# Optimization experiments

Hardware: AMD Instinct MI355X
Metric: run time of the kernel (lower is better)

Reference implementation:

```python
import jax, jax.numpy as jnp
import numpy as np

D_MODEL = 1024
D_STATE = 16
EXPAND = 2
D_INNER = D_MODEL * EXPAND          # 2048
DT_RANK = (D_MODEL + 15) // 16      # 64 (auto)
BATCH = 2
SEQ = 1024


def setup_inputs() -> dict:
    key = jax.random.key(0)
    ks = jax.random.split(key, 8)
    def nrm(k, shape, scale):
        return jax.random.normal(k, shape, dtype=jnp.float32) * scale
    x = jax.random.normal(ks[0], (BATCH, SEQ, D_MODEL), dtype=jnp.float32)
    W_in = nrm(ks[1], (D_MODEL, 2 * D_INNER), D_MODEL ** -0.5)
    W_conv = nrm(ks[2], (D_INNER, 3), 3 ** -0.5)           # depthwise kernel, taps [t-2,t-1,t]
    W_x = nrm(ks[3], (D_INNER, DT_RANK + 2 * D_STATE), D_INNER ** -0.5)
    W_dt = nrm(ks[4], (DT_RANK, D_INNER), DT_RANK ** -0.5)
    b_dt = nrm(ks[5], (D_INNER,), 0.1)
    # A_log init exactly as in the torch module: log(arange(1..d_state)) per channel
    A_log = jnp.log(jnp.tile(jnp.arange(1, D_STATE + 1, dtype=jnp.float32), (D_INNER, 1)))
    D_param = jnp.ones((D_INNER,), dtype=jnp.float32)
    W_out = nrm(ks[6], (D_INNER, D_MODEL), D_INNER ** -0.5)
    return {"x": x, "W_in": W_in, "W_conv": W_conv, "W_x": W_x,
            "W_dt": W_dt, "b_dt": b_dt, "A_log": A_log, "D_param": D_param,
            "W_out": W_out}


def _s6_forward(x, W_in, W_conv, W_x, W_dt, b_dt, A_log, D_param, W_out):
    B, L, _ = x.shape
    # input projection -> (u, res)
    u, res = jnp.split(x @ W_in, 2, axis=-1)           # each [B, L, d_inner]
    # depthwise causal conv, kernel=3, left pad 2 (matches Conv1d(pad=2)[..., :L])
    up = jnp.pad(u, ((0, 0), (2, 0), (0, 0)))
    u = (up[:, :L] * W_conv[:, 0]
         + up[:, 1:L + 1] * W_conv[:, 1]
         + up[:, 2:L + 2] * W_conv[:, 2])
    u = jax.nn.silu(u)
    # input-dependent SSM params
    x_dbl = u @ W_x                                     # [B, L, dt_rank + 2*d_state]
    dt, Bm, Cm = jnp.split(x_dbl, [DT_RANK, DT_RANK + D_STATE], axis=-1)
    delta = jax.nn.softplus(dt @ W_dt + b_dt)           # [B, L, d_inner]
    A = -jnp.exp(A_log)                                 # [d_inner, d_state]
    deltaA = jnp.exp(jnp.einsum('bld,dn->bldn', delta, A))     # [B, L, D, N]
    deltaB_u = jnp.einsum('bld,bln->bldn', delta * u, Bm)      # [B, L, D, N]
    # sequential selective scan over L via lax.scan
    def step(h, inp):
        dA, dbu, c = inp                # dA,dbu: [B,D,N], c: [B,N]
        h = dA * h + dbu
        y = jnp.einsum('bdn,bn->bd', h, c)
        return h, y
    h0 = jnp.zeros((B, D_INNER, D_STATE), dtype=u.dtype)
    _, ys = jax.lax.scan(step, h0, (jnp.moveaxis(deltaA, 1, 0),
                                    jnp.moveaxis(deltaB_u, 1, 0),
                                    jnp.moveaxis(Cm, 1, 0)))
    y = jnp.moveaxis(ys, 0, 1)                          # [B, L, d_inner]
    y = y + u * D_param
    y = y * jax.nn.silu(res)
    return y @ W_out                                    # [B, L, d_model]


def reference(x, W_in, W_conv, W_x, W_dt, b_dt, A_log, D_param, W_out):
    return _s6_forward(x, W_in, W_conv, W_x, W_dt, b_dt, A_log, D_param, W_out)
```

## Files before the change

kernel.cpp:

```cpp
#include <hip/hip_runtime.h>
#include <math.h>
#include <stdint.h>

#define BATCH 2
#define SEQ   1024
#define DM    1024
#define DI    2048
#define DS    16
#define DTR   64
#define ROWS  (BATCH*SEQ)
#define CH    32
#define NCH   (SEQ/CH)
#define NSPLIT 16
#define G4SPLIT 4

typedef unsigned short u16;
typedef __bf16 bf16x8 __attribute__((ext_vector_type(8)));
typedef float  f32x4  __attribute__((ext_vector_type(4)));
typedef short  short8 __attribute__((ext_vector_type(8)));
typedef short  short4v __attribute__((ext_vector_type(4)));

__device__ __forceinline__ float bf2f(u16 v) {
    return __uint_as_float(((unsigned)v) << 16);
}
__device__ __forceinline__ u16 f2bf(float f) {
    unsigned u = __float_as_uint(f);
    return (u16)((u + 0x7FFFu + ((u >> 16) & 1u)) >> 16);
}
__device__ __forceinline__ float softplus_f(float v) {
    return fmaxf(v, 0.f) + __logf(1.f + __expf(-fabsf(v)));
}
__device__ __forceinline__ float silu_f(float v) {
    return v / (1.f + __expf(-v));
}

__device__ __forceinline__ void gload16(const void* g, const void* l) {
    __builtin_amdgcn_global_load_lds(
        (const __attribute__((address_space(1))) unsigned int*)(uintptr_t)g,
        (__attribute__((address_space(3))) unsigned int*)(uintptr_t)l,
        16, 0, 0);
}

template<int EPI, typename TOUT>
__global__ __launch_bounds__(256) void gemm_bf16(
    const u16* __restrict__ A,
    const u16* __restrict__ BT,
    TOUT* __restrict__ C, u16* __restrict__ C2,
    int ldc, int N, int Ksplit, long long zCstride,
    const float* __restrict__ bias)
{
    __shared__ u16 As[2][128 * 64];
    __shared__ u16 Bs[2][128 * 64];

    const int K = (int)gridDim.z * Ksplit;
    int tid  = threadIdx.x;
    int lane = tid & 63, wid = tid >> 6;
    int wr = wid >> 1, wc = wid & 1;
    int row0 = blockIdx.y * 128, col0 = blockIdx.x * 128;
    int kbeg = blockIdx.z * Ksplit;
    const int niter = Ksplit >> 6;

    int sRow = wid * 32 + (lane >> 3);
    int sCol = (((lane & 7) ^ ((lane >> 3) & 7))) * 8;

    const u16* Abase = A  + (size_t)(row0 + sRow) * K + sCol;
    const u16* Bbase = BT + (size_t)(col0 + sRow) * K + sCol;

    int frow = lane & 15;
    int s0   = lane >> 4;
    int r7   = lane & 7;

    f32x4 acc[4][4] = {};

#define STAGE(buf, kk)                                                          \
    do {                                                                        \
        _Pragma("unroll")                                                       \
        for (int c = 0; c < 4; ++c) {                                           \
            gload16(Abase + (size_t)c * 8 * K + (kk),                           \
                    As[buf] + (wid * 32 + c * 8) * 64);                         \
            gload16(Bbase + (size_t)c * 8 * K + (kk),                           \
                    Bs[buf] + (wid * 32 + c * 8) * 64);                         \
        }                                                                       \
    } while (0)

    STAGE(0, kbeg);

    for (int i = 0; i < niter; ++i) {
        __syncthreads();
        int cur = i & 1;
        if (i + 1 < niter) STAGE(cur ^ 1, kbeg + (i + 1) * 64);

        #pragma unroll
        for (int kk = 0; kk < 2; ++kk) {
            bf16x8 af[4], bfr[4];
            #pragma unroll
            for (int m = 0; m < 4; ++m) {
                int row = wr * 64 + m * 16 + frow;
                int off = row * 64 + (((kk * 4 + s0) ^ r7) * 8);
                af[m] = *(const bf16x8*)(As[cur] + off);
            }
            #pragma unroll
            for (int n = 0; n < 4; ++n) {
                int row = wc * 64 + n * 16 + frow;
                int off = row * 64 + (((kk * 4 + s0) ^ r7) * 8);
                bfr[n] = *(const bf16x8*)(Bs[cur] + off);
            }
            #pragma unroll
            for (int m = 0; m < 4; ++m)
                #pragma unroll
                for (int n = 0; n < 4; ++n)
                    acc[m][n] = __builtin_amdgcn_mfma_f32_16x16x32_bf16(
                        af[m], bfr[n], acc[m][n], 0, 0, 0);
        }
    }
#undef STAGE

    int orow = row0 + wr * 64 + (lane >> 4) * 4;
    int ocol = col0 + wc * 64 + (lane & 15);

    if (EPI == 1) {
        bool isres = (col0 >= 2048);
        u16* dst = isres ? C2 : (u16*)C;
        int cb0 = ocol - (isres ? 2048 : 0);
        #pragma unroll
        for (int m = 0; m < 4; ++m)
            #pragma unroll
            for (int n = 0; n < 4; ++n) {
                int col = cb0 + n * 16;
                int roww = orow + m * 16;
                u16 tmp[4];
                #pragma unroll
                for (int r = 0; r < 4; ++r) {
                    float v = acc[m][n][r];
                    tmp[r] = f2bf(isres ? silu_f(v) : v);
                }
                *(short4v*)(dst + (size_t)col * ROWS + roww) = *(short4v*)tmp;
            }
    } else if (EPI == 2) {
        #pragma unroll
        for (int m = 0; m < 4; ++m)
            #pragma unroll
            for (int n = 0; n < 4; ++n) {
                int col = ocol + n * 16;
                int roww = orow + m * 16;
                float bv = bias[col];
                u16 tmp[4];
                #pragma unroll
                for (int r = 0; r < 4; ++r)
                    tmp[r] = f2bf(softplus_f(acc[m][n][r] + bv));
                *(short4v*)((u16*)C + (size_t)col * ROWS + roww) = *(short4v*)tmp;
            }
    } else {
        size_t zoff = (size_t)blockIdx.z * (size_t)zCstride;
        #pragma unroll
        for (int m = 0; m < 4; ++m)
            #pragma unroll
            for (int n = 0; n < 4; ++n) {
                int colb = ocol + n * 16;
                if (colb < N) {
                    #pragma unroll
                    for (int r = 0; r < 4; ++r) {
                        float v = acc[m][n][r];
                        size_t o = zoff + (size_t)(orow + m * 16 + r) * ldc + colb;
                        if constexpr (sizeof(TOUT) == 2) C[o] = (TOUT)f2bf(v);
                        else                             C[o] = (TOUT)v;
                    }
                }
            }
    }
}

__global__ __launch_bounds__(256) void tcast_kernel(
    const float* __restrict__ in, u16* __restrict__ outp,
    int K, int N, int Npad)
{
    __shared__ float tile[32][33];
    int tx = threadIdx.x & 31;
    int ty = threadIdx.x >> 5;
    int k0 = blockIdx.y * 32, n0 = blockIdx.x * 32;
    #pragma unroll
    for (int i = 0; i < 4; ++i) {
        int k = k0 + ty + i * 8, n = n0 + tx;
        tile[ty + i * 8][tx] = (k < K && n < N) ? in[(size_t)k * N + n] : 0.f;
    }
    __syncthreads();
    #pragma unroll
    for (int i = 0; i < 4; ++i) {
        int n = n0 + ty + i * 8, k = k0 + tx;
        if (n < Npad && k < K)
            outp[(size_t)n * K + k] = f2bf(tile[tx][ty + i * 8]);
    }
}

__global__ __launch_bounds__(256) void tbf_kernel(
    const u16* __restrict__ in, u16* __restrict__ outp, int R, int C)
{
    __shared__ u16 t[64][66];
    int tx = threadIdx.x & 63, ty = threadIdx.x >> 6;
    int r0 = blockIdx.y * 64, c0 = blockIdx.x * 64;
    #pragma unroll
    for (int i = 0; i < 16; ++i) {
        int r = ty + i * 4;
        t[r][tx] = in[(size_t)(r0 + r) * C + c0 + tx];
    }
    __syncthreads();
    #pragma unroll
    for (int i = 0; i < 16; ++i) {
        int r = ty + i * 4;
        outp[(size_t)(c0 + r) * R + r0 + tx] = t[tx][r];
    }
}

__global__ __launch_bounds__(256) void cast_kernel(
    const float* __restrict__ in, u16* __restrict__ outp, int n)
{
    int i = (blockIdx.x * 256 + threadIdx.x) * 4;
    if (i < n) {
        float4 v = *(const float4*)(in + i);
        outp[i + 0] = f2bf(v.x); outp[i + 1] = f2bf(v.y);
        outp[i + 2] = f2bf(v.z); outp[i + 3] = f2bf(v.w);
    }
}

__global__ __launch_bounds__(256) void reduce_split_kernel(
    const float* __restrict__ part, float* __restrict__ xdbl,
    u16* __restrict__ dtbf)
{
    int i = blockIdx.x * 256 + threadIdx.x;
    if (i < ROWS * 96) {
        float s = 0.f;
        #pragma unroll
        for (int z = 0; z < NSPLIT; ++z) s += part[(size_t)z * ROWS * 96 + i];
        xdbl[i] = s;
        int row = i / 96, col = i - row * 96;
        if (col < 64) dtbf[row * 64 + col] = f2bf(s);
    }
}

__global__ __launch_bounds__(256) void reduce4_kernel(
    const float* __restrict__ part, float* __restrict__ outp)
{
    int i = (blockIdx.x * 256 + threadIdx.x) * 4;
    const size_t S = (size_t)ROWS * 1024;
    float4 a = *(const float4*)(part + i);
    float4 b = *(const float4*)(part + S + i);
    float4 c = *(const float4*)(part + 2 * S + i);
    float4 d = *(const float4*)(part + 3 * S + i);
    float4 o;
    o.x = a.x + b.x + c.x + d.x;
    o.y = a.y + b.y + c.y + d.y;
    o.z = a.z + b.z + c.z + d.z;
    o.w = a.w + b.w + c.w + d.w;
    *(float4*)(outp + i) = o;
}

__global__ __launch_bounds__(256) void conv_silu_kernel(
    const u16* __restrict__ upreT,
    const float* __restrict__ Wc,
    u16* __restrict__ uT)
{
    int gt = blockIdx.x * 256 + threadIdx.x;
    int rb = gt & (ROWS / 8 - 1);
    int d  = gt >> 8;
    int r0 = rb * 8;
    int l0 = r0 & (SEQ - 1);
    const u16* rowp = upreT + (size_t)d * ROWS + r0;
    short8 cur = *(const short8*)rowp;
    float w0 = Wc[d * 3 + 0], w1 = Wc[d * 3 + 1], w2 = Wc[d * 3 + 2];
    float pm1 = (l0 > 0) ? bf2f(rowp[-1]) : 0.f;
    float pm2 = (l0 > 0) ? bf2f(rowp[-2]) : 0.f;
    float c[8];
    #pragma unroll
    for (int j = 0; j < 8; ++j) c[j] = bf2f((u16)cur[j]);
    short8 o;
    o[0] = (short)f2bf(silu_f(w2 * c[0] + w1 * pm1 + w0 * pm2));
    o[1] = (short)f2bf(silu_f(w2 * c[1] + w1 * c[0] + w0 * pm1));
    #pragma unroll
    for (int j = 2; j < 8; ++j)
        o[j] = (short)f2bf(silu_f(w2 * c[j] + w1 * c[j - 1] + w0 * c[j - 2]));
    *(short8*)(uT + (size_t)d * ROWS + r0) = o;
}

__global__ __launch_bounds__(256) void scan_chunk_kernel(
    const u16*  __restrict__ dvT,
    const u16*  __restrict__ uT,
    const float* __restrict__ xdbl,
    const float* __restrict__ A_log,
    float* __restrict__ P,
    float* __restrict__ Q)
{
    int gtid = blockIdx.x * 256 + threadIdx.x;
    int nq = gtid & 3;
    int d  = (gtid >> 2) & (DI - 1);
    int rc = gtid >> 13;
    int chunk = rc & (NCH - 1);
    int b = rc >> 5;

    float4 a4 = *(const float4*)(A_log + (size_t)d * DS + nq * 4);
    float Av[4] = {-__expf(a4.x), -__expf(a4.y), -__expf(a4.z), -__expf(a4.w)};
    float h[4] = {};
    float dsum = 0.f;

    int r0 = b * SEQ + chunk * CH;
    const u16* drow = dvT + (size_t)d * ROWS + r0;
    const u16* urow = uT  + (size_t)d * ROWS + r0;
    const float* xrow = xdbl + (size_t)r0 * 96 + 64 + nq * 4;

    #pragma unroll
    for (int half = 0; half < 2; ++half) {
        short8 dv8[2], u8[2];
        #pragma unroll
        for (int q = 0; q < 2; ++q) {
            dv8[q] = *(const short8*)(drow + half * 16 + q * 8);
            u8[q]  = *(const short8*)(urow + half * 16 + q * 8);
        }
        #pragma unroll
        for (int j = 0; j < 16; ++j) {
            int l = half * 16 + j;
            float dv = bf2f((u16)dv8[j >> 3][j & 7]);
            float du = dv * bf2f((u16)u8[j >> 3][j & 7]);
            dsum += dv;
            float4 b4 = *(const float4*)(xrow + l * 96);
            h[0] = __expf(dv * Av[0]) * h[0] + du * b4.x;
            h[1] = __expf(dv * Av[1]) * h[1] + du * b4.y;
            h[2] = __expf(dv * Av[2]) * h[2] + du * b4.z;
            h[3] = __expf(dv * Av[3]) * h[3] + du * b4.w;
        }
    }
    size_t off = ((size_t)(b * NCH + chunk) * DI + d) * DS + nq * 4;
    float4 p4 = {__expf(dsum * Av[0]), __expf(dsum * Av[1]),
                 __expf(dsum * Av[2]), __expf(dsum * Av[3])};
    *(float4*)(P + off) = p4;
    *(float4*)(Q + off) = make_float4(h[0], h[1], h[2], h[3]);
}

__global__ __launch_bounds__(256) void scan_combine_kernel(
    const float* __restrict__ P,
    float* __restrict__ Q)
{
    int idx = blockIdx.x * 256 + threadIdx.x;
    int nd = idx & (DI * DS - 1);
    int b = idx >> 15;
    float h = 0.f;
    for (int c = 0; c < NCH; ++c) {
        size_t off = (size_t)(b * NCH + c) * DI * DS + nd;
        float p = P[off], q = Q[off];
        Q[off] = h;
        h = p * h + q;
    }
}

__global__ __launch_bounds__(256) void scan_final_kernel(
    const u16*  __restrict__ dvT,
    const u16*  __restrict__ uT,
    const float* __restrict__ xdbl,
    const float* __restrict__ A_log,
    const float* __restrict__ hin,
    const u16*  __restrict__ resT,
    const float* __restrict__ Dp,
    u16* __restrict__ yT)
{
    int gtid = blockIdx.x * 256 + threadIdx.x;
    int nq = gtid & 3;
    int d  = (gtid >> 2) & (DI - 1);
    int rc = gtid >> 13;
    int chunk = rc & (NCH - 1);
    int b = rc >> 5;

    float4 a4 = *(const float4*)(A_log + (size_t)d * DS + nq * 4);
    float Av[4] = {-__expf(a4.x), -__expf(a4.y), -__expf(a4.z), -__expf(a4.w)};
    size_t off = ((size_t)(b * NCH + chunk) * DI + d) * DS + nq * 4;
    float4 h4 = *(const float4*)(hin + off);
    float h[4] = {h4.x, h4.y, h4.z, h4.w};
    float Dd = Dp[d];

    int r0 = b * SEQ + chunk * CH;
    const u16* drow = dvT  + (size_t)d * ROWS + r0;
    const u16* urow = uT   + (size_t)d * ROWS + r0;
    const u16* rrow = resT + (size_t)d * ROWS + r0;
    const float* xrow = xdbl + (size_t)r0 * 96 + 64 + nq * 4;
    u16* yrow = yT + (size_t)d * ROWS + r0;

    #pragma unroll
    for (int half = 0; half < 2; ++half) {
        short8 dv8[2], u8[2], r8[2];
        #pragma unroll
        for (int q = 0; q < 2; ++q) {
            dv8[q] = *(const short8*)(drow + half * 16 + q * 8);
            u8[q]  = *(const short8*)(urow + half * 16 + q * 8);
            r8[q]  = *(const short8*)(rrow + half * 16 + q * 8);
        }
        short8 o8;
        #pragma unroll
        for (int j = 0; j < 16; ++j) {
            int l = half * 16 + j;
            float dv = bf2f((u16)dv8[j >> 3][j & 7]);
            float uv = bf2f((u16)u8[j >> 3][j & 7]);
            float du = dv * uv;
            float4 b4 = *(const float4*)(xrow + l * 96);
            float4 c4 = *(const float4*)(xrow + l * 96 + 16);
            h[0] = __expf(dv * Av[0]) * h[0] + du * b4.x;
            h[1] = __expf(dv * Av[1]) * h[1] + du * b4.y;
            h[2] = __expf(dv * Av[2]) * h[2] + du * b4.z;
            h[3] = __expf(dv * Av[3]) * h[3] + du * b4.w;
            float y = h[0] * c4.x + h[1] * c4.y + h[2] * c4.z + h[3] * c4.w;
            y += __shfl_xor(y, 1);
            y += __shfl_xor(y, 2);
            float v = (y + uv * Dd) * bf2f((u16)r8[j >> 3][j & 7]);
            o8[j & 7] = (short)f2bf(v);
            if ((j & 7) == 7 && nq == 0)
                *(short8*)(yrow + half * 16 + (j & ~7)) = o8;
        }
    }
}

extern "C" void kernel_launch(void* const* d_in, const int* in_sizes, int n_in,
                              void* d_out, int out_size, void* d_ws, size_t ws_size,
                              hipStream_t stream) {
    const float* x       = (const float*)d_in[0];
    const float* W_in    = (const float*)d_in[1];
    const float* W_conv  = (const float*)d_in[2];
    const float* W_x     = (const float*)d_in[3];
    const float* W_dt    = (const float*)d_in[4];
    const float* b_dt    = (const float*)d_in[5];
    const float* A_log   = (const float*)d_in[6];
    const float* D_param = (const float*)d_in[7];
    const float* W_out   = (const float*)d_in[8];
    float* out = (float*)d_out;

    float* buf0  = (float*)d_ws;
    float* D16   = buf0 + (size_t)ROWS * 4096;
    float* Qbuf  = D16 + (size_t)ROWS * DI;
    float* R1    = Qbuf + (size_t)BATCH * NCH * DI * DS;
    float* R2    = R1 + 2 * 1024 * 1024;
    float* xdbl  = R2 + 1024 * 1024;
    u16*  uT     = (u16*)(xdbl + (size_t)ROWS * 96);
    u16*  WxT    = (u16*)(uT + (size_t)ROWS * DI);

    u16* u_preT = (u16*)D16;
    u16* resT   = (u16*)D16 + (size_t)ROWS * DI;
    u16* dvT    = (u16*)D16;
    u16* WinT  = (u16*)R1;
    u16* WdtT  = (u16*)R1;
    u16* dtbf  = (u16*)R1 + 2048 * 64;
    float* P   = R1;
    u16* yT    = (u16*)R1;
    float* Xpart  = buf0;
    u16* u_row    = (u16*)(buf0 + 4 * 1024 * 1024);
    float* G4part = buf0;
    u16* y_row    = (u16*)Qbuf;
    u16* xbf   = (u16*)R2;
    u16* WoutT = (u16*)R2;

    dim3 blk(256);

    tcast_kernel<<<dim3(4096/32, 1024/32), blk, 0, stream>>>(W_in, WinT, 1024, 4096, 4096);
    cast_kernel<<<(ROWS * DM / 4 + 255) / 256, blk, 0, stream>>>(x, xbf, ROWS * DM);

    gemm_bf16<1, u16><<<dim3(4096/128, ROWS/128, 1), blk, 0, stream>>>(
        xbf, WinT, u_preT, resT, 0, 4096, 1024, 0, nullptr);

    tcast_kernel<<<dim3(1024/32, 2048/32), blk, 0, stream>>>(W_out, WoutT, 2048, 1024, 1024);
    tcast_kernel<<<dim3(2048/32, 64/32), blk, 0, stream>>>(W_dt, WdtT, 64, 2048, 2048);
    tcast_kernel<<<dim3(128/32, 2048/32), blk, 0, stream>>>(W_x, WxT, 2048, 96, 128);

    conv_silu_kernel<<<(ROWS * DI / 8) / 256, blk, 0, stream>>>(u_preT, W_conv, uT);

    tbf_kernel<<<dim3(ROWS/64, DI/64), blk, 0, stream>>>(uT, u_row, DI, ROWS);

    gemm_bf16<0, float><<<dim3(1, ROWS/128, NSPLIT), blk, 0, stream>>>(
        u_row, WxT, Xpart, nullptr, 96, 96, DI / NSPLIT, (long long)ROWS * 96, nullptr);
    reduce_split_kernel<<<(ROWS * 96 + 255) / 256, blk, 0, stream>>>(Xpart, xdbl, dtbf);

    gemm_bf16<2, u16><<<dim3(DI/128, ROWS/128, 1), blk, 0, stream>>>(
        dtbf, WdtT, dvT, nullptr, 0, DI, DTR, 0, b_dt);

    scan_chunk_kernel<<<(BATCH * NCH * DI * 4) / 256, blk, 0, stream>>>(
        dvT, uT, xdbl, A_log, P, Qbuf);
    scan_combine_kernel<<<(BATCH * DI * DS) / 256, blk, 0, stream>>>(P, Qbuf);
    scan_final_kernel<<<(BATCH * NCH * DI * 4) / 256, blk, 0, stream>>>(
        dvT, uT, xdbl, A_log, Qbuf, resT, D_param, yT);

    tbf_kernel<<<dim3(ROWS/64, DI/64), blk, 0, stream>>>(yT, y_row, DI, ROWS);

    gemm_bf16<0, float><<<dim3(1024/128, ROWS/128, G4SPLIT), blk, 0, stream>>>(
        y_row, WoutT, G4part, nullptr, 1024, 1024, 2048 / G4SPLIT, (long long)ROWS * 1024, nullptr);
    reduce4_kernel<<<(ROWS * 1024 / 4) / 256, blk, 0, stream>>>(G4part, out);
}
```

Baseline: 148.9 us.

## Fuse chunked scan, combine, and final pass into one kernel using LDS

Replaces the three-kernel chunked selective scan (chunk summaries, a global combine, a final pass) with one kernel. Each block owns two (batch, channel) units across all 32 chunks and keeps the chunk P/Q summaries in shared memory. A 32-thread sequential combine runs in LDS between two barriers. This removes two launches and the global P/Q round trips, but most threads sit idle during the serial combine.

```diff
diff --git a/kernel.cpp b/kernel.cpp
--- a/kernel.cpp
+++ b/kernel.cpp
@@ -281,104 +281,83 @@
     *(short8*)(uT + (size_t)d * ROWS + r0) = o;
 }
 
-__global__ __launch_bounds__(256) void scan_chunk_kernel(
+__global__ __launch_bounds__(256) void scan_fused_kernel(
     const u16*  __restrict__ dvT,
     const u16*  __restrict__ uT,
     const float* __restrict__ xdbl,
     const float* __restrict__ A_log,
-    float* __restrict__ P,
-    float* __restrict__ Q)
-{
-    int gtid = blockIdx.x * 256 + threadIdx.x;
-    int nq = gtid & 3;
-    int d  = (gtid >> 2) & (DI - 1);
-    int rc = gtid >> 13;
-    int chunk = rc & (NCH - 1);
-    int b = rc >> 5;
+    const u16*  __restrict__ resT,
+    const float* __restrict__ Dp,
+    u16* __restrict__ yT)
+{
+    __shared__ float lP[2][NCH][DS];
+    __shared__ float lQ[2][NCH][DS];
+
+    int tid = threadIdx.x;
+    int nq = tid & 3;
+    int chunk = (tid >> 2) & (NCH - 1);
+    int du = tid >> 7;
+    int unit = blockIdx.x * 2 + du;
+    int d = unit & (DI - 1);
+    int b = unit >> 11;
 
     float4 a4 = *(const float4*)(A_log + (size_t)d * DS + nq * 4);
     float Av[4] = {-__expf(a4.x), -__expf(a4.y), -__expf(a4.z), -__expf(a4.w)};
-    float h[4] = {};
-    float dsum = 0.f;
 
     int r0 = b * SEQ + chunk * CH;
     const u16* drow = dvT + (size_t)d * ROWS + r0;
     const u16* urow = uT  + (size_t)d * ROWS + r0;
     const float* xrow = xdbl + (size_t)r0 * 96 + 64 + nq * 4;
 
-    #pragma unroll
-    for (int half = 0; half < 2; ++half) {
-        short8 dv8[2], u8[2];
-        #pragma unroll
-        for (int q = 0; q < 2; ++q) {
-            dv8[q] = *(const short8*)(drow + half * 16 + q * 8);
-            u8[q]  = *(const short8*)(urow + half * 16 + q * 8);
-        }
-        #pragma unroll
-        for (int j = 0; j < 16; ++j) {
-            int l = half * 16 + j;
-            float dv = bf2f((u16)dv8[j >> 3][j & 7]);
-            float du = dv * bf2f((u16)u8[j >> 3][j & 7]);
-            dsum += dv;
-            float4 b4 = *(const float4*)(xrow + l * 96);
-            h[0] = __expf(dv * Av[0]) * h[0] + du * b4.x;
-            h[1] = __expf(dv * Av[1]) * h[1] + du * b4.y;
-            h[2] = __expf(dv * Av[2]) * h[2] + du * b4.z;
-            h[3] = __expf(dv * Av[3]) * h[3] + du * b4.w;
-        }
-    }
-    size_t off = ((size_t)(b * NCH + chunk) * DI + d) * DS + nq * 4;
-    float4 p4 = {__expf(dsum * Av[0]), __expf(dsum * Av[1]),
-                 __expf(dsum * Av[2]), __expf(dsum * Av[3])};
-    *(float4*)(P + off) = p4;
-    *(float4*)(Q + off) = make_float4(h[0], h[1], h[2], h[3]);
-}
-
-__global__ __launch_bounds__(256) void scan_combine_kernel(
-    const float* __restrict__ P,
-    float* __restrict__ Q)
-{
-    int idx = blockIdx.x * 256 + threadIdx.x;
-    int nd = idx & (DI * DS - 1);
-    int b = idx >> 15;
-    float h = 0.f;
-    for (int c = 0; c < NCH; ++c) {
-        size_t off = (size_t)(b * NCH + c) * DI * DS + nd;
-        float p = P[off], q = Q[off];
-        Q[off] = h;
-        h = p * h + q;
-    }
-}
-
-__global__ __launch_bounds__(256) void scan_final_kernel(
-    const u16*  __restrict__ dvT,
-    const u16*  __restrict__ uT,
-    const float* __restrict__ xdbl,
-    const float* __restrict__ A_log,
-    const float* __restrict__ hin,
-    const u16*  __restrict__ resT,
-    const float* __restrict__ Dp,
-    u16* __restrict__ yT)
-{
-    int gtid = blockIdx.x * 256 + threadIdx.x;
-    int nq = gtid & 3;
-    int d  = (gtid >> 2) & (DI - 1);
-    int rc = gtid >> 13;
-    int chunk = rc & (NCH - 1);
-    int b = rc >> 5;
-
-    float4 a4 = *(const float4*)(A_log + (size_t)d * DS + nq * 4);
-    float Av[4] = {-__expf(a4.x), -__expf(a4.y), -__expf(a4.z), -__expf(a4.w)};
-    size_t off = ((size_t)(b * NCH + chunk) * DI + d) * DS + nq * 4;
-    float4 h4 = *(const float4*)(hin + off);
-    float h[4] = {h4.x, h4.y, h4.z, h4.w};
+    {
+        float h[4] = {};
+        float dsum = 0.f;
+        #pragma unroll
+        for (int half = 0; half < 2; ++half) {
+            short8 dv8[2], u8[2];
+            #pragma unroll
+            for (int q = 0; q < 2; ++q) {
+                dv8[q] = *(const short8*)(drow + half * 16 + q * 8);
+                u8[q]  = *(const short8*)(urow + half * 16 + q * 8);
+            }
+            #pragma unroll
+            for (int j = 0; j < 16; ++j) {
+                int l = half * 16 + j;
+                float dv = bf2f((u16)dv8[j >> 3][j & 7]);
+                float duv = dv * bf2f((u16)u8[j >> 3][j & 7]);
+                dsum += dv;
+                float4 b4 = *(const float4*)(xrow + l * 96);
+                h[0] = __expf(dv * Av[0]) * h[0] + duv * b4.x;
+                h[1] = __expf(dv * Av[1]) * h[1] + duv * b4.y;
+                h[2] = __expf(dv * Av[2]) * h[2] + duv * b4.z;
+                h[3] = __expf(dv * Av[3]) * h[3] + duv * b4.w;
+            }
+        }
+        #pragma unroll
+        for (int k = 0; k < 4; ++k) {
+            lP[du][chunk][nq * 4 + k] = __expf(dsum * Av[k]);
+            lQ[du][chunk][nq * 4 + k] = h[k];
+        }
+    }
+    __syncthreads();
+
+    if (tid < 32) {
+        int cdu = tid >> 4, n = tid & 15;
+        float hh = 0.f;
+        #pragma unroll 4
+        for (int c = 0; c < NCH; ++c) {
+            float p = lP[cdu][c][n], q = lQ[cdu][c][n];
+            lQ[cdu][c][n] = hh;
+            hh = p * hh + q;
+        }
+    }
+    __syncthreads();
+
+    float h[4];
+    #pragma unroll
+    for (int k = 0; k < 4; ++k) h[k] = lQ[du][chunk][nq * 4 + k];
     float Dd = Dp[d];
-
-    int r0 = b * SEQ + chunk * CH;
-    const u16* drow = dvT  + (size_t)d * ROWS + r0;
-    const u16* urow = uT   + (size_t)d * ROWS + r0;
     const u16* rrow = resT + (size_t)d * ROWS + r0;
-    const float* xrow = xdbl + (size_t)r0 * 96 + 64 + nq * 4;
     u16* yrow = yT + (size_t)d * ROWS + r0;
 
     #pragma unroll
@@ -396,13 +375,13 @@
             int l = half * 16 + j;
             float dv = bf2f((u16)dv8[j >> 3][j & 7]);
             float uv = bf2f((u16)u8[j >> 3][j & 7]);
-            float du = dv * uv;
+            float duv = dv * uv;
             float4 b4 = *(const float4*)(xrow + l * 96);
             float4 c4 = *(const float4*)(xrow + l * 96 + 16);
-            h[0] = __expf(dv * Av[0]) * h[0] + du * b4.x;
-            h[1] = __expf(dv * Av[1]) * h[1] + du * b4.y;
-            h[2] = __expf(dv * Av[2]) * h[2] + du * b4.z;
-            h[3] = __expf(dv * Av[3]) * h[3] + du * b4.w;
+            h[0] = __expf(dv * Av[0]) * h[0] + duv * b4.x;
+            h[1] = __expf(dv * Av[1]) * h[1] + duv * b4.y;
+            h[2] = __expf(dv * Av[2]) * h[2] + duv * b4.z;
+            h[3] = __expf(dv * Av[3]) * h[3] + duv * b4.w;
             float y = h[0] * c4.x + h[1] * c4.y + h[2] * c4.z + h[3] * c4.w;
             y += __shfl_xor(y, 1);
             y += __shfl_xor(y, 2);
@@ -443,7 +422,6 @@
     u16* WinT  = (u16*)R1;
     u16* WdtT  = (u16*)R1;
     u16* dtbf  = (u16*)R1 + 2048 * 64;
-    float* P   = R1;
     u16* yT    = (u16*)R1;
     float* Xpart  = buf0;
     u16* u_row    = (u16*)(buf0 + 4 * 1024 * 1024);
@@ -475,11 +453,8 @@
     gemm_bf16<2, u16><<<dim3(DI/128, ROWS/128, 1), blk, 0, stream>>>(
         dtbf, WdtT, dvT, nullptr, 0, DI, DTR, 0, b_dt);
 
-    scan_chunk_kernel<<<(BATCH * NCH * DI * 4) / 256, blk, 0, stream>>>(
-        dvT, uT, xdbl, A_log, P, Qbuf);
-    scan_combine_kernel<<<(BATCH * DI * DS) / 256, blk, 0, stream>>>(P, Qbuf);
-    scan_final_kernel<<<(BATCH * NCH * DI * 4) / 256, blk, 0, stream>>>(
-        dvT, uT, xdbl, A_log, Qbuf, resT, D_param, yT);
+    scan_fused_kernel<<<(BATCH * DI) / 2, blk, 0, stream>>>(
+        dvT, uT, xdbl, A_log, resT, D_param, yT);
 
     tbf_kernel<<<dim3(ROWS/64, DI/64), blk, 0, stream>>>(yT, y_row, DI, ROWS);
 
```

Measured after the change: 142.8 us. -4.1%, faster.
